# Kernel tuning notes

Measured on AMD Instinct MI355X. Metric: run time of the kernel, lower is better.

## Reference

```python
import jax, jax.numpy as jnp
import numpy as np

B, N, NNZ = 512, 512, 8192
ENTITY, EMB, HID = 30000, 64, 100
PAD_ID = ENTITY - 1


def setup_inputs() -> dict:
    key = jax.random.key(0)
    ks = jax.random.split(key, 8)
    hyperneigh = jax.random.randint(ks[0], (B, N), 0, PAD_ID, dtype=jnp.int64)
    adj_rows = jax.random.randint(ks[1], (B, NNZ), 0, N, dtype=jnp.int32)
    adj_cols = jax.random.randint(ks[2], (B, NNZ), 0, N, dtype=jnp.int32)
    adj_vals = jax.random.uniform(ks[3], (B, NNZ), dtype=jnp.float32)
    emb_table = jax.random.normal(ks[4], (ENTITY, EMB), dtype=jnp.float32)
    emb_table = emb_table.at[PAD_ID].set(0.0)  # padding_idx row is zero
    stdv1 = 1.0 / np.sqrt(HID)
    W1 = jax.random.uniform(ks[5], (EMB, HID), minval=-stdv1, maxval=stdv1, dtype=jnp.float32)
    b1 = jax.random.uniform(ks[6], (HID,), minval=-stdv1, maxval=stdv1, dtype=jnp.float32)
    k7, k8 = jax.random.split(ks[7])
    W2 = jax.random.uniform(k7, (HID, HID), minval=-stdv1, maxval=stdv1, dtype=jnp.float32)
    b2 = jax.random.uniform(k8, (HID,), minval=-stdv1, maxval=stdv1, dtype=jnp.float32)
    return dict(hyperneigh=hyperneigh, adj_rows=adj_rows, adj_cols=adj_cols,
                adj_vals=adj_vals, emb_table=emb_table, W1=W1, b1=b1, W2=W2, b2=b2)


def _spmm(rows, cols, vals, X):
    # sparse [N,N] @ X[N,H] via gather + segment_sum (COO, fixed nnz)
    msgs = vals[:, None] * X[cols]  # [nnz, H]
    return jax.ops.segment_sum(msgs, rows, num_segments=N)

_batched_spmm = jax.vmap(_spmm, in_axes=(0, 0, 0, 0))


def reference(hyperneigh, adj_rows, adj_cols, adj_vals, emb_table, W1, b1, W2, b2):
    # embedding lookup: [B, N, EMB]
    x = emb_table[hyperneigh]
    # HGNN_conv layer 1: support = X @ W; out = A @ support + bias
    support = jnp.einsum('bne,eh->bnh', x, W1)
    x = _batched_spmm(adj_rows, adj_cols, adj_vals, support) + b1
    # HGNN_conv layer 2
    support = jnp.einsum('bnh,hk->bnk', x, W2)
    x = _batched_spmm(adj_rows, adj_cols, adj_vals, support) + b2
    return x  # [B, N, HID]
```

## Files before the change

kernel.cpp:

```cpp
#include <hip/hip_runtime.h>

#define BB   512
#define NN   512
#define NNZ  8192
#define EMB  64
#define HID  100
#define DUPC 0x7FFF
#define HTSZ 512

#define OFF_RC      0
#define OFF_VPK     16777216
#define OFF_SSTART  25165824
#define OFF_SUPT    26216448
#define OFF_W1T     84936704
#define OFF_W2T     84951040

typedef __attribute__((ext_vector_type(8))) short short8;
typedef __attribute__((ext_vector_type(4))) float floatx4;

__device__ __forceinline__ unsigned short f2bf(float f) {
    unsigned u = __float_as_uint(f);
    unsigned r = (u + 0x7fffu + ((u >> 16) & 1u)) >> 16;
    return (unsigned short)r;
}

__device__ __forceinline__ float bf2f(unsigned short b) {
    return __uint_as_float((unsigned)b << 16);
}

__device__ __forceinline__ short8 pack8(float4 a, float4 b) {
    short8 s;
    s[0] = (short)f2bf(a.x); s[1] = (short)f2bf(a.y);
    s[2] = (short)f2bf(a.z); s[3] = (short)f2bf(a.w);
    s[4] = (short)f2bf(b.x); s[5] = (short)f2bf(b.y);
    s[6] = (short)f2bf(b.z); s[7] = (short)f2bf(b.w);
    return s;
}

__device__ __forceinline__ int keyhash(int key) {
    return (int)(((unsigned)key * 2654435761u) >> 23) & (HTSZ - 1);
}

__device__ __forceinline__ size_t supt_addr(int batch, int col, int k) {
    return (size_t)batch * 57344 + (size_t)(k >> 5) * 3584 + (size_t)col * 32 + (k & 31);
}

__device__ __forceinline__ int ad_addr(int rr, int c) {
    return (rr >> 4) * 8192 + (c >> 5) * 512 + ((c >> 3) & 3) * 128 + (rr & 15) * 8 + (c & 7);
}

__global__ __launch_bounds__(512) void k_bucket(
    const int* __restrict__ rows, const int* __restrict__ cols,
    const float* __restrict__ vals, int* __restrict__ rc,
    unsigned short* __restrict__ vpk, int* __restrict__ sstart,
    const float* __restrict__ W1, const float* __restrict__ W2,
    unsigned short* __restrict__ w1t, unsigned short* __restrict__ w2t)
{
    __shared__ int      rl[NNZ];
    __shared__ unsigned ub[NN * 16];
    __shared__ int      wcnt[8][8];
    __shared__ int      wbase[8][8];
    __shared__ int      htk[HTSZ];
    __shared__ float    htv[HTSZ];

    unsigned short* vh = (unsigned short*)ub;

    const int b    = blockIdx.x;
    const int tid  = threadIdx.x;
    const int wave = tid >> 6;

    {
        int pid = b + (tid << 9);
        if (pid < 7168) {
            int h = pid >> 6, k = pid & 63;
            w1t[pid] = f2bf((h < 100) ? W1[k * 100 + h] : 0.f);
        } else if (pid < 7168 + 14336) {
            int id2 = pid - 7168;
            int h = id2 >> 7, k = id2 & 127;
            w2t[id2] = f2bf((h < 100 && k < 100) ? W2[k * 100 + h] : 0.f);
        }
    }

    const int*   rb = rows + (size_t)b * NNZ;
    const int*   cb = cols + (size_t)b * NNZ;
    const float* vb = vals + (size_t)b * NNZ;

    int rr[16], cc[16];
    float vv[16];
    #pragma unroll
    for (int i = 0; i < 16; ++i) {
        int idx = tid + i * 512;
        rr[i] = rb[idx]; cc[i] = cb[idx]; vv[i] = vb[idx];
    }

    #pragma unroll
    for (int i = 0; i < 16; ++i) ub[tid + i * 512] = 0u;
    htk[tid] = -1;
    htv[tid] = 0.f;
    if (tid < 64) ((int*)wcnt)[tid] = 0;
    __syncthreads();

    unsigned dupmask = 0;
    #pragma unroll
    for (int i = 0; i < 16; ++i) {
        unsigned bit = 1u << (cc[i] & 31);
        unsigned old = atomicOr(&ub[(rr[i] << 4) + (cc[i] >> 5)], bit);
        if (old & bit) {
            dupmask |= 1u << i;
            int key = (rr[i] << 16) | cc[i];
            int h = keyhash(key);
            bool placed = false;
            for (int p = 0; p < HTSZ; ++p) {
                int prev = atomicCAS(&htk[h], -1, key);
                if (prev == -1 || prev == key) { placed = true; break; }
                h = (h + 1) & (HTSZ - 1);
            }
            if (placed) atomicAdd(&htv[h], vv[i]);
            else        dupmask &= ~(1u << i);
        }
        atomicAdd(&wcnt[wave][rr[i] >> 6], 1);
    }
    __syncthreads();

    if (tid == 0) {
        int acc = 0;
        #pragma unroll
        for (int s = 0; s < 8; ++s) {
            sstart[b * 9 + s] = acc;
            #pragma unroll
            for (int w = 0; w < 8; ++w) { wbase[w][s] = acc; acc += wcnt[w][s]; }
        }
        sstart[b * 9 + 8] = NNZ;
    }
    __syncthreads();
    if (tid < 64) ((int*)wcnt)[tid] = ((int*)wbase)[tid];
    __syncthreads();

    #pragma unroll
    for (int i = 0; i < 16; ++i) {
        int s = rr[i] >> 6;
        int pos = atomicAdd(&wcnt[wave][s], 1);
        bool dup = (dupmask >> i) & 1;
        float v = vv[i];
        if (!dup) {
            int key = (rr[i] << 16) | cc[i];
            int h = keyhash(key);
            for (int p = 0; p < HTSZ; ++p) {
                int k2 = htk[h];
                if (k2 == -1) break;
                if (k2 == key) { v += htv[h]; break; }
                h = (h + 1) & (HTSZ - 1);
            }
        }
        rl[pos] = (rr[i] << 16) | (dup ? DUPC : cc[i]);
        vh[pos] = dup ? 0 : f2bf(v);
    }
    __syncthreads();

    {
        int* orc = rc + (size_t)b * NNZ;
        #pragma unroll
        for (int i = 0; i < 16; ++i) {
            int idx = tid + i * 512;
            orc[idx] = rl[idx];
        }
        unsigned* ov = (unsigned*)(vpk + (size_t)b * NNZ);
        #pragma unroll
        for (int i = 0; i < 8; ++i) {
            int p = tid + i * 512;
            ov[p] = (unsigned)vh[2 * p] | ((unsigned)vh[2 * p + 1] << 16);
        }
    }
}

__global__ __launch_bounds__(256) void k_gemm1_mfma(
    const int* __restrict__ hyper, const float* __restrict__ emb,
    const unsigned short* __restrict__ w1t, unsigned short* __restrict__ supT)
{
    const int lane = threadIdx.x & 63, wave = threadIdx.x >> 6;
    const int l15 = lane & 15, g4 = lane >> 4;

    short8 bq[7][2];
    #pragma unroll
    for (int ct = 0; ct < 7; ++ct)
        #pragma unroll
        for (int kt = 0; kt < 2; ++kt)
            bq[ct][kt] = *(const short8*)(w1t + (ct * 16 + l15) * 64 + kt * 32 + g4 * 8);

    const int wsid = blockIdx.x * 4 + wave;
    #pragma unroll 2
    for (int i = 0; i < 4; ++i) {
        const int  rb   = wsid * 4 + i;
        const long base = (long)rb * 16;
        const int  rid  = hyper[base + l15];
        const float* ep = emb + (long)rid * EMB + g4 * 8;
        float4 f0 = *(const float4*)(ep);
        float4 f1 = *(const float4*)(ep + 4);
        float4 f2 = *(const float4*)(ep + 32);
        float4 f3 = *(const float4*)(ep + 36);
        short8 a0 = pack8(f0, f1);
        short8 a1 = pack8(f2, f3);

        floatx4 acc[7];
        #pragma unroll
        for (int ct = 0; ct < 7; ++ct) acc[ct] = (floatx4)0.f;
        #pragma unroll
        for (int ct = 0; ct < 7; ++ct) {
            acc[ct] = __builtin_amdgcn_mfma_f32_16x16x32_bf16(a0, bq[ct][0], acc[ct], 0, 0, 0);
            acc[ct] = __builtin_amdgcn_mfma_f32_16x16x32_bf16(a1, bq[ct][1], acc[ct], 0, 0, 0);
        }

        const int batch = rb >> 5;
        const int inrow = (rb & 31) * 16 + g4 * 4;
        #pragma unroll
        for (int ct = 0; ct < 7; ++ct) {
            int col = ct * 16 + l15;
            uint2 w;
            w.x = (unsigned)f2bf(acc[ct][0]) | ((unsigned)f2bf(acc[ct][1]) << 16);
            w.y = (unsigned)f2bf(acc[ct][2]) | ((unsigned)f2bf(acc[ct][3]) << 16);
            *(uint2*)(supT + supt_addr(batch, col, inrow)) = w;
        }
    }
}

__global__ __launch_bounds__(256) void k_gemm2_mfma(
    const unsigned short* __restrict__ h1, const unsigned short* __restrict__ w2t,
    unsigned short* __restrict__ supT)
{
    const int lane = threadIdx.x & 63, wave = threadIdx.x >> 6;
    const int l15 = lane & 15, g4 = lane >> 4;
    const int ct0 = (wave & 1) ? 4 : 0;

    short8 bq[4][4];
    #pragma unroll
    for (int ctl = 0; ctl < 4; ++ctl) {
        int ct = ct0 + ctl;
        if (ct < 7)
            #pragma unroll
            for (int kt = 0; kt < 4; ++kt)
                bq[ctl][kt] = *(const short8*)(w2t + (ct * 16 + l15) * 128 + kt * 32 + g4 * 8);
    }

    const int wp = blockIdx.x * 2 + (wave >> 1);
    #pragma unroll 2
    for (int i = 0; i < 8; ++i) {
        const int  rb   = wp * 8 + i;
        const long base = (long)rb * 16;
        const unsigned short* rp = h1 + (size_t)(base + l15) * 112;

        short8 a[4];
        #pragma unroll
        for (int kt = 0; kt < 4; ++kt) {
            int k0 = kt * 32 + g4 * 8;
            short8 av = (short8)(short)0;
            if (k0 < 112) av = *(const short8*)(rp + k0);
            a[kt] = av;
        }

        floatx4 acc[4];
        #pragma unroll
        for (int ctl = 0; ctl < 4; ++ctl) acc[ctl] = (floatx4)0.f;
        #pragma unroll
        for (int ctl = 0; ctl < 4; ++ctl) {
            if (ct0 + ctl < 7) {
                #pragma unroll
                for (int kt = 0; kt < 4; ++kt)
                    acc[ctl] = __builtin_amdgcn_mfma_f32_16x16x32_bf16(a[kt], bq[ctl][kt], acc[ctl], 0, 0, 0);
            }
        }

        const int batch = rb >> 5;
        const int inrow = (rb & 31) * 16 + g4 * 4;
        #pragma unroll
        for (int ctl = 0; ctl < 4; ++ctl) {
            if (ct0 + ctl < 7) {
                int col = (ct0 + ctl) * 16 + l15;
                uint2 w;
                w.x = (unsigned)f2bf(acc[ctl][0]) | ((unsigned)f2bf(acc[ctl][1]) << 16);
                w.y = (unsigned)f2bf(acc[ctl][2]) | ((unsigned)f2bf(acc[ctl][3]) << 16);
                *(uint2*)(supT + supt_addr(batch, col, inrow)) = w;
            }
        }
    }
}

template<bool FINAL>
__global__ __launch_bounds__(512, 4) void k_spmm_mfma(
    const int* __restrict__ sstart, const int* __restrict__ rc,
    const unsigned short* __restrict__ vpk, const unsigned short* __restrict__ supT,
    const float* __restrict__ bias, unsigned short* __restrict__ h1,
    float* __restrict__ out)
{
    __shared__ unsigned short Ad[64 * 512];

    const int tid    = threadIdx.x;
    const int xcd    = blockIdx.x & 7;
    const int local  = blockIdx.x >> 3;
    const int batch  = xcd * 64 + (local >> 3);
    const int stripe = local & 7;
    const int r0     = stripe * 64;

    const int lane = tid & 63, wave = tid >> 6;
    const int l15 = lane & 15, g4 = lane >> 4;
    const int ng  = wave & 3, kh = wave >> 2;
    const int nt0 = ng * 2;
    const bool two = (nt0 + 1) < 7;
    const int ktb = kh * 8;

    const int s0 = sstart[batch * 9 + stripe];
    const int e0 = sstart[batch * 9 + stripe + 1];
    const int*            rcb = rc + (size_t)batch * NNZ;
    const unsigned short* vvb = vpk + (size_t)batch * NNZ;
    int            pc[3];
    unsigned short pv[3];
    #pragma unroll
    for (int i = 0; i < 3; ++i) {
        int idx = s0 + tid + i * 512;
        bool ok = idx < e0;
        pc[i] = ok ? rcb[idx] : 0;
        pv[i] = ok ? vvb[idx] : 0;
    }

    const unsigned short* b0p = supT + (size_t)batch * 57344 + (size_t)ktb * 3584
                               + (nt0 * 16 + l15) * 32 + g4 * 8;
    const unsigned short* b1p = b0p + 512;
    short8 bfr[16];
    #pragma unroll
    for (int kt = 0; kt < 8; ++kt) {
        bfr[2 * kt] = *(const short8*)(b0p + (size_t)kt * 3584);
        if (two) bfr[2 * kt + 1] = *(const short8*)(b1p + (size_t)kt * 3584);
        else     bfr[2 * kt + 1] = (short8)(short)0;
    }

    {
        uint4* z = (uint4*)Ad;
        #pragma unroll
        for (int i = 0; i < 8; ++i) z[tid + i * 512] = make_uint4(0u, 0u, 0u, 0u);
    }
    __syncthreads();

    #pragma unroll
    for (int i = 0; i < 3; ++i) {
        int idx = s0 + tid + i * 512;
        if (idx < e0) {
            int rr = ((pc[i] >> 16) & 0xffff) - r0;
            int c  = pc[i] & 0xffff;
            if (c < 512) Ad[ad_addr(rr, c)] = pv[i];
        }
    }
    for (int idx = s0 + 1536 + tid; idx < e0; idx += 512) {
        int p = rcb[idx];
        int rr = ((p >> 16) & 0xffff) - r0;
        int c  = p & 0xffff;
        if (c < 512) Ad[ad_addr(rr, c)] = vvb[idx];
    }
    __syncthreads();

    const unsigned short* ap = Ad + (size_t)ktb * 512 + lane * 8;

    floatx4 acc[2][4];
    #pragma unroll
    for (int n = 0; n < 2; ++n)
        #pragma unroll
        for (int m = 0; m < 4; ++m) acc[n][m] = (floatx4)0.f;

    #pragma unroll
    for (int kt = 0; kt < 8; ++kt) {
        #pragma unroll
        for (int m = 0; m < 4; ++m) {
            short8 a = *(const short8*)(ap + m * 8192 + kt * 512);
            acc[0][m] = __builtin_amdgcn_mfma_f32_16x16x32_bf16(a, bfr[2 * kt], acc[0][m], 0, 0, 0);
            if (two)
                acc[1][m] = __builtin_amdgcn_mfma_f32_16x16x32_bf16(a, bfr[2 * kt + 1], acc[1][m], 0, 0, 0);
        }
    }
    __syncthreads();

    float* redu = (float*)Ad;
    if (kh == 1) {
        #pragma unroll
        for (int nn = 0; nn < 2; ++nn)
            #pragma unroll
            for (int m = 0; m < 4; ++m)
                #pragma unroll
                for (int q = 0; q < 4; ++q)
                    redu[ng * 2048 + ((nn * 4 + m) * 4 + q) * 64 + lane] = acc[nn][m][q];
    }
    __syncthreads();

    if (kh == 0) {
        #pragma unroll
        for (int nn = 0; nn < 2; ++nn)
            #pragma unroll
            for (int m = 0; m < 4; ++m)
                #pragma unroll
                for (int q = 0; q < 4; ++q)
                    acc[nn][m][q] += redu[ng * 2048 + ((nn * 4 + m) * 4 + q) * 64 + lane];

        if (FINAL) {
            float* st = (float*)((char*)Ad + 32768);
            #pragma unroll
            for (int nn = 0; nn < 2; ++nn) {
                int nt = nt0 + nn;
                if (nt >= 7) break;
                int col = nt * 16 + l15;
                float bi = (col < HID) ? bias[col] : 0.f;
                #pragma unroll
                for (int m = 0; m < 4; ++m) {
                    int row = m * 16 + g4 * 4;
                    #pragma unroll
                    for (int q = 0; q < 4; ++q)
                        st[(row + q) * 112 + col] = acc[nn][m][q] + bi;
                }
            }
        } else {
            unsigned short* st = (unsigned short*)((char*)Ad + 32768);
            #pragma unroll
            for (int nn = 0; nn < 2; ++nn) {
                int nt = nt0 + nn;
                if (nt >= 7) break;
                int col = nt * 16 + l15;
                float bi = (col < HID) ? bias[col] : 0.f;
                #pragma unroll
                for (int m = 0; m < 4; ++m) {
                    int row = m * 16 + g4 * 4;
                    #pragma unroll
                    for (int q = 0; q < 4; ++q)
                        st[(row + q) * 112 + col] = f2bf(acc[nn][m][q] + bi);
                }
            }
        }
    }
    __syncthreads();

    if (FINAL) {
        const float* st = (const float*)((char*)Ad + 32768);
        #pragma unroll
        for (int i = 0; i < 4; ++i) {
            int flat = tid + i * 512;
            if (flat < 1600) {
                int row = flat / 25, wi = flat - row * 25;
                float4 v = *(const float4*)(st + row * 112 + wi * 4);
                *(float4*)(out + ((size_t)batch * NN + r0 + row) * HID + wi * 4) = v;
            }
        }
    } else {
        const unsigned short* st = (const unsigned short*)((char*)Ad + 32768);
        #pragma unroll
        for (int i = 0; i < 2; ++i) {
            int flat = tid + i * 512;
            if (flat < 896) {
                int row = flat / 14, wi = flat - row * 14;
                uint4 v = *(const uint4*)(st + row * 112 + wi * 8);
                *(uint4*)(h1 + ((size_t)batch * NN + r0 + row) * 112 + wi * 8) = v;
            }
        }
    }
}

extern "C" void kernel_launch(void* const* d_in, const int* in_sizes, int n_in,
                              void* d_out, int out_size, void* d_ws, size_t ws_size,
                              hipStream_t stream)
{
    const int*   hyper = (const int*)  d_in[0];
    const int*   arows = (const int*)  d_in[1];
    const int*   acols = (const int*)  d_in[2];
    const float* avals = (const float*)d_in[3];
    const float* emb   = (const float*)d_in[4];
    const float* W1    = (const float*)d_in[5];
    const float* b1    = (const float*)d_in[6];
    const float* W2    = (const float*)d_in[7];
    const float* b2    = (const float*)d_in[8];

    float*          out = (float*)d_out;
    unsigned short* h1  = (unsigned short*)d_out;
    char*           ws  = (char*)d_ws;

    int*            rc     = (int*)           (ws + OFF_RC);
    unsigned short* vpk    = (unsigned short*)(ws + OFF_VPK);
    int*            sstart = (int*)           (ws + OFF_SSTART);
    unsigned short* supT   = (unsigned short*)(ws + OFF_SUPT);
    unsigned short* w1t    = (unsigned short*)(ws + OFF_W1T);
    unsigned short* w2t    = (unsigned short*)(ws + OFF_W2T);

    k_bucket<<<BB, 512, 0, stream>>>(arows, acols, avals, rc, vpk, sstart,
                                     W1, W2, w1t, w2t);

    k_gemm1_mfma<<<1024, 256, 0, stream>>>(hyper, emb, w1t, supT);
    k_spmm_mfma<false><<<BB * 8, 512, 0, stream>>>(sstart, rc, vpk, supT, b1, h1, out);
    k_gemm2_mfma<<<1024, 256, 0, stream>>>(h1, w2t, supT);
    k_spmm_mfma<true><<<BB * 8, 512, 0, stream>>>(sstart, rc, vpk, supT, b2, h1, out);
}
```

Measured before the change: 197.3 us.

## Fuse second-layer GEMM into first SpMM epilogue, dropping k_gemm2 kernel

The first SpMM kernel now multiplies its 64-row bf16 output tile, staged in shared memory, by W2 with MFMA and writes the layer-2 support directly in the transposed supT layout. This removes the separate k_gemm2 launch and the round trip of h1 through global memory. gemm1 now writes its support into the output buffer, and the second SpMM reads from a workspace buffer. The shared-memory stride is padded to 116, and the extra MFMA work and W2 loads in the epilogue add register pressure and latency to the SpMM kernel.

```diff
diff --git a/kernel.cpp b/kernel.cpp
--- a/kernel.cpp
+++ b/kernel.cpp
@@ -11,7 +11,7 @@
 #define OFF_RC      0
 #define OFF_VPK     16777216
 #define OFF_SSTART  25165824
-#define OFF_SUPT    26216448
+#define OFF_SUPT2   26216448
 #define OFF_W1T     84936704
 #define OFF_W2T     84951040
 
@@ -223,73 +223,12 @@
     }
 }
 
-__global__ __launch_bounds__(256) void k_gemm2_mfma(
-    const unsigned short* __restrict__ h1, const unsigned short* __restrict__ w2t,
-    unsigned short* __restrict__ supT)
-{
-    const int lane = threadIdx.x & 63, wave = threadIdx.x >> 6;
-    const int l15 = lane & 15, g4 = lane >> 4;
-    const int ct0 = (wave & 1) ? 4 : 0;
-
-    short8 bq[4][4];
-    #pragma unroll
-    for (int ctl = 0; ctl < 4; ++ctl) {
-        int ct = ct0 + ctl;
-        if (ct < 7)
-            #pragma unroll
-            for (int kt = 0; kt < 4; ++kt)
-                bq[ctl][kt] = *(const short8*)(w2t + (ct * 16 + l15) * 128 + kt * 32 + g4 * 8);
-    }
-
-    const int wp = blockIdx.x * 2 + (wave >> 1);
-    #pragma unroll 2
-    for (int i = 0; i < 8; ++i) {
-        const int  rb   = wp * 8 + i;
-        const long base = (long)rb * 16;
-        const unsigned short* rp = h1 + (size_t)(base + l15) * 112;
-
-        short8 a[4];
-        #pragma unroll
-        for (int kt = 0; kt < 4; ++kt) {
-            int k0 = kt * 32 + g4 * 8;
-            short8 av = (short8)(short)0;
-            if (k0 < 112) av = *(const short8*)(rp + k0);
-            a[kt] = av;
-        }
-
-        floatx4 acc[4];
-        #pragma unroll
-        for (int ctl = 0; ctl < 4; ++ctl) acc[ctl] = (floatx4)0.f;
-        #pragma unroll
-        for (int ctl = 0; ctl < 4; ++ctl) {
-            if (ct0 + ctl < 7) {
-                #pragma unroll
-                for (int kt = 0; kt < 4; ++kt)
-                    acc[ctl] = __builtin_amdgcn_mfma_f32_16x16x32_bf16(a[kt], bq[ctl][kt], acc[ctl], 0, 0, 0);
-            }
-        }
-
-        const int batch = rb >> 5;
-        const int inrow = (rb & 31) * 16 + g4 * 4;
-        #pragma unroll
-        for (int ctl = 0; ctl < 4; ++ctl) {
-            if (ct0 + ctl < 7) {
-                int col = (ct0 + ctl) * 16 + l15;
-                uint2 w;
-                w.x = (unsigned)f2bf(acc[ctl][0]) | ((unsigned)f2bf(acc[ctl][1]) << 16);
-                w.y = (unsigned)f2bf(acc[ctl][2]) | ((unsigned)f2bf(acc[ctl][3]) << 16);
-                *(uint2*)(supT + supt_addr(batch, col, inrow)) = w;
-            }
-        }
-    }
-}
-
 template<bool FINAL>
 __global__ __launch_bounds__(512, 4) void k_spmm_mfma(
     const int* __restrict__ sstart, const int* __restrict__ rc,
-    const unsigned short* __restrict__ vpk, const unsigned short* __restrict__ supT,
-    const float* __restrict__ bias, unsigned short* __restrict__ h1,
-    float* __restrict__ out)
+    const unsigned short* __restrict__ vpk, const unsigned short* __restrict__ supIn,
+    const unsigned short* __restrict__ w2t, const float* __restrict__ bias,
+    unsigned short* __restrict__ supOut, float* __restrict__ out)
 {
     __shared__ unsigned short Ad[64 * 512];
 
@@ -321,7 +260,7 @@
         pv[i] = ok ? vvb[idx] : 0;
     }
 
-    const unsigned short* b0p = supT + (size_t)batch * 57344 + (size_t)ktb * 3584
+    const unsigned short* b0p = supIn + (size_t)batch * 57344 + (size_t)ktb * 3584
                                + (nt0 * 16 + l15) * 32 + g4 * 8;
     const unsigned short* b1p = b0p + 512;
     short8 bfr[16];
@@ -426,7 +365,7 @@
                     int row = m * 16 + g4 * 4;
                     #pragma unroll
                     for (int q = 0; q < 4; ++q)
-                        st[(row + q) * 112 + col] = f2bf(acc[nn][m][q] + bi);
+                        st[(row + q) * 116 + col] = f2bf(acc[nn][m][q] + bi);
                 }
             }
         }
@@ -446,13 +385,47 @@
         }
     } else {
         const unsigned short* st = (const unsigned short*)((char*)Ad + 32768);
-        #pragma unroll
-        for (int i = 0; i < 2; ++i) {
-            int flat = tid + i * 512;
-            if (flat < 896) {
-                int row = flat / 14, wi = flat - row * 14;
-                uint4 v = *(const uint4*)(st + row * 112 + wi * 8);
-                *(uint4*)(h1 + ((size_t)batch * NN + r0 + row) * 112 + wi * 8) = v;
+        const int mh  = wave >> 2;
+        const int ng2 = wave & 3;
+        const int n0  = ng2 * 2;
+        const bool two2 = (n0 + 1) < 7;
+
+        floatx4 a2[2][2];
+        #pragma unroll
+        for (int mi = 0; mi < 2; ++mi)
+            #pragma unroll
+            for (int ni = 0; ni < 2; ++ni) a2[mi][ni] = (floatx4)0.f;
+
+        #pragma unroll
+        for (int kt2 = 0; kt2 < 4; ++kt2) {
+            short8 b0 = *(const short8*)(w2t + (n0 * 16 + l15) * 128 + kt2 * 32 + g4 * 8);
+            short8 b1 = (short8)(short)0;
+            if (two2) b1 = *(const short8*)(w2t + ((n0 + 1) * 16 + l15) * 128 + kt2 * 32 + g4 * 8);
+            #pragma unroll
+            for (int mi = 0; mi < 2; ++mi) {
+                int mt = mh * 2 + mi;
+                short8 a = *(const short8*)(st + (mt * 16 + l15) * 116 + kt2 * 32 + g4 * 8);
+                a2[mi][0] = __builtin_amdgcn_mfma_f32_16x16x32_bf16(a, b0, a2[mi][0], 0, 0, 0);
+                if (two2)
+                    a2[mi][1] = __builtin_amdgcn_mfma_f32_16x16x32_bf16(a, b1, a2[mi][1], 0, 0, 0);
+            }
+        }
+
+        #pragma unroll
+        for (int mi = 0; mi < 2; ++mi) {
+            int mt = mh * 2 + mi;
+            int lr = mt * 16 + g4 * 4;
+            size_t kta = (size_t)batch * 57344 + (size_t)(2 * stripe + (lr >> 5)) * 3584;
+            int kin = lr & 31;
+            #pragma unroll
+            for (int ni = 0; ni < 2; ++ni) {
+                int nt = n0 + ni;
+                if (nt >= 7) break;
+                int col = nt * 16 + l15;
+                uint2 w;
+                w.x = (unsigned)f2bf(a2[mi][ni][0]) | ((unsigned)f2bf(a2[mi][ni][1]) << 16);
+                w.y = (unsigned)f2bf(a2[mi][ni][2]) | ((unsigned)f2bf(a2[mi][ni][3]) << 16);
+                *(uint2*)(supOut + kta + (size_t)col * 32 + kin) = w;
             }
         }
     }
@@ -472,22 +445,23 @@
     const float* W2    = (const float*)d_in[7];
     const float* b2    = (const float*)d_in[8];
 
-    float*          out = (float*)d_out;
-    unsigned short* h1  = (unsigned short*)d_out;
-    char*           ws  = (char*)d_ws;
+    float*          out   = (float*)d_out;
+    unsigned short* supT1 = (unsigned short*)d_out;
+    char*           ws    = (char*)d_ws;
 
     int*            rc     = (int*)           (ws + OFF_RC);
     unsigned short* vpk    = (unsigned short*)(ws + OFF_VPK);
     int*            sstart = (int*)           (ws + OFF_SSTART);
-    unsigned short* supT   = (unsigned short*)(ws + OFF_SUPT);
+    unsigned short* supT2  = (unsigned short*)(ws + OFF_SUPT2);
     unsigned short* w1t    = (unsigned short*)(ws + OFF_W1T);
     unsigned short* w2t    = (unsigned short*)(ws + OFF_W2T);
 
     k_bucket<<<BB, 512, 0, stream>>>(arows, acols, avals, rc, vpk, sstart,
                                      W1, W2, w1t, w2t);
 
-    k_gemm1_mfma<<<1024, 256, 0, stream>>>(hyper, emb, w1t, supT);
-    k_spmm_mfma<false><<<BB * 8, 512, 0, stream>>>(sstart, rc, vpk, supT, b1, h1, out);
-    k_gemm2_mfma<<<1024, 256, 0, stream>>>(h1, w2t, supT);
-    k_spmm_mfma<true><<<BB * 8, 512, 0, stream>>>(sstart, rc, vpk, supT, b2, h1, out);
-}
+    k_gemm1_mfma<<<1024, 256, 0, stream>>>(hyper, emb, w1t, supT1);
+    k_spmm_mfma<false><<<BB * 8, 512, 0, stream>>>(sstart, rc, vpk, supT1, w2t,
+                                                   b1, supT2, out);
+    k_spmm_mfma<true><<<BB * 8, 512, 0, stream>>>(sstart, rc, vpk, supT2, w2t,
+                                                  b2, supT2, out);
+}
```

Result: slower. 201.7 us (+2.2%).
